# Performance work log

Hardware: AMD Instinct MI355X
Metric: run time of the kernel (lower is better)

## Reference

```python
import jax, jax.numpy as jnp
import numpy as np

ALPHA = 4.0  # spikingjelly surrogate.Sigmoid default
TAU = 2.0    # LIFNode default

@jax.custom_vjp
def spike(x):
    return (x >= 0).astype(x.dtype)

def _spike_fwd(x):
    return spike(x), x

def _spike_bwd(x, g):
    s = jax.nn.sigmoid(ALPHA * x)
    return (g * ALPHA * s * (1.0 - s),)

spike.defvjp(_spike_fwd, _spike_bwd)

def lif(x_seq, v_th):
    # multi-step LIF over leading time dim; decay_input=True, v_reset=0 (hard reset)
    def step(v, x):
        v = v + (x - v) / TAU
        s = spike(v - v_th)
        return v * (1.0 - s), s
    _, s_seq = jax.lax.scan(step, jnp.zeros_like(x_seq[0]), x_seq)
    return s_seq

def bn_c(x, gamma, beta, mean, var, eps=1e-5):
    # eval-mode BatchNorm1d over channel axis 2 of [T,N,C,V]
    inv = (gamma / jnp.sqrt(var + eps))[None, None, :, None]
    return (x - mean[None, None, :, None]) * inv + beta[None, None, :, None]

def conv1x1(x, w):
    # 1x1 Conv1d == channel mixing: w [Cout,Cin], x [T,N,C,V]
    return jnp.einsum('oc,tncv->tnov', w, x)

def setup_inputs() -> dict:
    key = jax.random.key(0)
    T, N, C, V = 4, 512, 256, 25
    ks = jax.random.split(key, 24)
    def bn_params(k1, k2, k3, k4):
        return (jax.random.uniform(k1, (C,)) * 0.5 + 0.75,
                jax.random.normal(k2, (C,)) * 0.1,
                jax.random.normal(k3, (C,)) * 0.1,
                jax.random.uniform(k4, (C,)) * 0.5 + 0.5)
    x = jax.random.normal(ks[0], (T, N, C, V), dtype=jnp.float32)
    s = 1.0 / np.sqrt(C)
    wq = jax.random.normal(ks[1], (C, C)) * s
    wk = jax.random.normal(ks[2], (C, C)) * s
    wv = jax.random.normal(ks[3], (C, C)) * s
    wp = jax.random.normal(ks[4], (C, C)) * s
    bp = jax.random.normal(ks[5], (C,)) * 0.02
    qg, qb, qm, qvar = bn_params(ks[6], ks[7], ks[8], ks[9])
    kg, kb, km, kvar = bn_params(ks[10], ks[11], ks[12], ks[13])
    vg, vb, vm, vvar = bn_params(ks[14], ks[15], ks[16], ks[17])
    pg, pb, pm, pvar = bn_params(ks[18], ks[19], ks[20], ks[21])
    return dict(x=x, wq=wq, wk=wk, wv=wv, wp=wp, bp=bp,
                qg=qg, qb=qb, qm=qm, qvar=qvar,
                kg=kg, kb=kb, km=km, kvar=kvar,
                vg=vg, vb=vb, vm=vm, vvar=vvar,
                pg=pg, pb=pb, pm=pm, pvar=pvar)

def reference(x, wq, wk, wv, wp, bp, qg, qb, qm, qvar, kg, kb, km, kvar,
              vg, vb, vm, vvar, pg, pb, pm, pvar):
    T, N, C, V = x.shape
    H = 8
    D = C // H
    scale = 0.125

    def branch(w, g, b, m, var):
        s = lif(bn_c(conv1x1(x, w), g, b, m, var), 1.0)       # [T,N,C,V]
        # -> [T,N,V,C] -> [T,N,V,H,D] -> [T,N,H,V,D]
        return jnp.transpose(s, (0, 1, 3, 2)).reshape(T, N, V, H, D).transpose(0, 1, 3, 2, 4)

    q = branch(wq, qg, qb, qm, qvar)
    k = branch(wk, kg, kb, km, kvar)
    v = branch(wv, vg, vb, vm, vvar)

    attn = jnp.einsum('tnhvd,tnhwd->tnhvw', q, k)            # binary spike attn, no softmax
    y = jnp.einsum('tnhvw,tnhwd->tnhvd', attn, v) * scale    # [T,N,H,V,D]
    y = y.transpose(0, 1, 2, 4, 3).reshape(T, N, C, V)       # transpose(3,4) then merge H*D=C
    y = lif(y, 0.5)                                          # attn_lif, v_threshold=0.5
    y = conv1x1(y, wp) + bp[None, None, :, None]             # proj_conv (bias=True)
    y = lif(bn_c(y, pg, pb, pm, pvar), 1.0)                  # proj_bn + proj_lif
    return y + x                                             # residual
```

## Files before the change

### kernel.cpp

```cpp
#include <hip/hip_runtime.h>
#include <cstdint>
#include <cstddef>

#define T_ 4
#define N_ 512
#define C_ 256
#define V_ 25
#define H_ 8

typedef _Float16 half8_t __attribute__((ext_vector_type(8)));
typedef float f32x16 __attribute__((ext_vector_type(16)));

__device__ __forceinline__ f32x16 mfma16(half8_t a, half8_t b, f32x16 c) {
  return __builtin_amdgcn_mfma_f32_32x32x16_f16(a, b, c, 0, 0, 0);
}

__global__ void kw_stage(const float* __restrict__ wq, const float* __restrict__ wk,
                         const float* __restrict__ wv, const float* __restrict__ wp,
                         const float* __restrict__ qg, const float* __restrict__ qvar,
                         const float* __restrict__ kg, const float* __restrict__ kvar,
                         const float* __restrict__ vg, const float* __restrict__ vvar,
                         const float* __restrict__ pg, const float* __restrict__ pvar,
                         _Float16* __restrict__ Wstg) {
  int i = blockIdx.x * 512 + threadIdx.x;
  int j = i & 7, lane = (i >> 3) & 63, rt = (i >> 9) & 3, m = (i >> 11) & 1;
  int s = (i >> 12) & 3, p = (i >> 14) & 3, c = i >> 16;
  int kt = p * 4 + s;
  int row = rt * 32 + (lane & 31);
  int k = kt * 16 + (lane >> 5) * 8 + j;
  const float *w, *g, *va;
  int grow;
  if (c < 6) {
    int br = c >> 1;
    w = br == 0 ? wq : br == 1 ? wk : wv;
    g = br == 0 ? qg : br == 1 ? kg : vg;
    va = br == 0 ? qvar : br == 1 ? kvar : vvar;
    grow = (c & 1) * 128 + row;
  } else {
    w = wp; g = pg; va = pvar;
    grow = (c - 6) * 128 + row;
  }
  float sc = g[grow] / sqrtf(va[grow] + 1e-5f);
  float wv_ = w[grow * 256 + k] * sc;
  _Float16 hi = (_Float16)wv_;
  Wstg[i] = (m == 0) ? hi : (_Float16)(wv_ - (float)hi);
}

__global__ void kx_stage(const float* __restrict__ x, _Float16* __restrict__ X16) {
  __shared__ float Xt[256 * 28];
  const int n = blockIdx.x, tid = threadIdx.x;
  for (int t = 0; t < 4; ++t) {
    __syncthreads();
    for (int i = tid; i < 6400; i += 256) {
      int k = i / 25, v = i - k * 25;
      Xt[k * 28 + v] = x[(size_t)(t * N_ + n) * 6400 + i];
    }
    __syncthreads();
    for (int jj = tid; jj < 800; jj += 256) {
      int kt = jj / 50, r = jj - kt * 50;
      int v = r >> 1, lkg = r & 1;
      int k0 = kt * 16 + lkg * 8;
      half8_t hi, lo;
#pragma unroll
      for (int e = 0; e < 8; ++e) {
        float f = Xt[(k0 + e) * 28 + v];
        _Float16 h = (_Float16)f;
        hi[e] = h;
        lo[e] = (_Float16)(f - (float)h);
      }
      int col = t * 25 + v;
      size_t bhi = ((((size_t)n * 2 + 0) * 16 + kt) * 100 + col) * 16 + lkg * 8;
      size_t blo = ((((size_t)n * 2 + 1) * 16 + kt) * 100 + col) * 16 + lkg * 8;
      *(half8_t*)(X16 + bhi) = hi;
      *(half8_t*)(X16 + blo) = lo;
    }
  }
}

#define STAGE_A(gidx, bufsel)                                                     \
  do {                                                                            \
    const _Float16* sp_ = Wstg + (size_t)(gidx) * 16384 + tid * 8;                \
    char* dp_ = Abuf + (bufsel) * 32768 + tid * 16;                               \
    __builtin_amdgcn_global_load_lds((const uint32_t*)(sp_),          (uint32_t*)(dp_),          16, 0, 0); \
    __builtin_amdgcn_global_load_lds((const uint32_t*)(sp_ + 4096),   (uint32_t*)(dp_ + 8192),   16, 0, 0); \
    __builtin_amdgcn_global_load_lds((const uint32_t*)(sp_ + 8192),   (uint32_t*)(dp_ + 16384),  16, 0, 0); \
    __builtin_amdgcn_global_load_lds((const uint32_t*)(sp_ + 12288),  (uint32_t*)(dp_ + 24576),  16, 0, 0); \
  } while (0)

#define MS_BYTE(colx, rowx) ((colx) * 256 + (((rowx) * 4) ^ (((colx) & 7) << 4)))

__launch_bounds__(512, 2)
__global__ void k1_mfma(const _Float16* __restrict__ X16, const _Float16* __restrict__ Wstg,
                        const float* __restrict__ qg, const float* __restrict__ qb,
                        const float* __restrict__ qm, const float* __restrict__ qvar,
                        const float* __restrict__ kg, const float* __restrict__ kb,
                        const float* __restrict__ km, const float* __restrict__ kvar,
                        const float* __restrict__ vg, const float* __restrict__ vb,
                        const float* __restrict__ vm, const float* __restrict__ vvar,
                        uint32_t* __restrict__ masks) {
  __shared__ __align__(16) char LDSb[65536 + 32768 + 512];
  char* Abuf = LDSb;
  char* MsB = LDSb + 65536;
  float* bic = (float*)(LDSb + 65536 + 32768);

  const int n = blockIdx.x, tid = threadIdx.x;
  const int lane = tid & 63, wid = tid >> 6;
  const int ks = wid & 1, cp = (wid >> 1) & 1, rt2 = wid >> 2;
  const int lr = lane & 31, lkg = lane >> 5;

  half8_t Bh[16], Bl[16];
#pragma unroll
  for (int ct = 0; ct < 2; ++ct) {
    int col = cp * 64 + ct * 32 + lr;
    if (col > 99) col = 99;
#pragma unroll
    for (int ktl = 0; ktl < 8; ++ktl) {
      int kt = ktl * 2 + ks;
      Bh[ct * 8 + ktl] = *(const half8_t*)(X16 + ((((size_t)n * 2 + 0) * 16 + kt) * 100 + col) * 16 + lkg * 8);
      Bl[ct * 8 + ktl] = *(const half8_t*)(X16 + ((((size_t)n * 2 + 1) * 16 + kt) * 100 + col) * 16 + lkg * 8);
    }
  }
  STAGE_A(0, 0);

  for (int c = 0; c < 6; ++c) {
    const int br = c >> 1;
    f32x16 acc00 = {}, acc01 = {}, acc10 = {}, acc11 = {};
#pragma unroll
    for (int p = 0; p < 4; ++p) {
      __syncthreads();
      if (p == 0 && tid < 128) {
        int ch = (c & 1) * 128 + tid;
        const float* g  = br == 0 ? qg : br == 1 ? kg : vg;
        const float* be = br == 0 ? qb : br == 1 ? kb : vb;
        const float* mu = br == 0 ? qm : br == 1 ? km : vm;
        const float* va = br == 0 ? qvar : br == 1 ? kvar : vvar;
        float sc = g[ch] / sqrtf(va[ch] + 1e-5f);
        bic[tid] = be[ch] - mu[ch] * sc;
      }
      int gnext = c * 4 + p + 1;
      if (gnext < 24) STAGE_A(gnext, (p + 1) & 1);
#pragma unroll
      for (int s2 = 0; s2 < 2; ++s2) {
        const int s = s2 * 2 + ks;
        const int bi = p * 2 + s2;
        const char* kb = Abuf + (p & 1) * 32768 + s * 8192 + (rt2 * 2) * 1024 + lane * 16;
        half8_t Ah0 = *(const half8_t*)(kb);
        half8_t Ah1 = *(const half8_t*)(kb + 1024);
        half8_t Al0 = *(const half8_t*)(kb + 4096);
        half8_t Al1 = *(const half8_t*)(kb + 4096 + 1024);
        __builtin_amdgcn_s_setprio(1);
        acc00 = mfma16(Ah0, Bh[bi], acc00);
        acc01 = mfma16(Ah0, Bh[8 + bi], acc01);
        acc10 = mfma16(Ah1, Bh[bi], acc10);
        acc11 = mfma16(Ah1, Bh[8 + bi], acc11);
        acc00 = mfma16(Ah0, Bl[bi], acc00);
        acc01 = mfma16(Ah0, Bl[8 + bi], acc01);
        acc10 = mfma16(Ah1, Bl[bi], acc10);
        acc11 = mfma16(Ah1, Bl[8 + bi], acc11);
        acc00 = mfma16(Al0, Bh[bi], acc00);
        acc01 = mfma16(Al0, Bh[8 + bi], acc01);
        acc10 = mfma16(Al1, Bh[bi], acc10);
        acc11 = mfma16(Al1, Bh[8 + bi], acc11);
        __builtin_amdgcn_s_setprio(0);
      }
    }

    __syncthreads();
    if (ks == 0) {
#pragma unroll
      for (int rsub = 0; rsub < 2; ++rsub) {
#pragma unroll
        for (int ct = 0; ct < 2; ++ct) {
          int col = cp * 64 + ct * 32 + lr;
          if (col < 100) {
            f32x16 A = rsub ? (ct ? acc11 : acc10) : (ct ? acc01 : acc00);
#pragma unroll
            for (int qq = 0; qq < 4; ++qq) {
              int rowb = (rt2 * 2 + rsub) * 32 + qq * 8 + lkg * 4;
              *(float4*)(MsB + MS_BYTE(col, rowb)) =
                  make_float4(A[qq * 4], A[qq * 4 + 1], A[qq * 4 + 2], A[qq * 4 + 3]);
            }
          }
        }
      }
    }
    __syncthreads();
    if (ks == 1) {
#pragma unroll
      for (int rsub = 0; rsub < 2; ++rsub) {
#pragma unroll
        for (int ct = 0; ct < 2; ++ct) {
          int col = cp * 64 + ct * 32 + lr;
          if (col < 100) {
            f32x16 A = rsub ? (ct ? acc11 : acc10) : (ct ? acc01 : acc00);
#pragma unroll
            for (int qq = 0; qq < 4; ++qq) {
              int rowb = (rt2 * 2 + rsub) * 32 + qq * 8 + lkg * 4;
              float4* mp = (float4*)(MsB + MS_BYTE(col, rowb));
              float4 old = *mp;
              *mp = make_float4(old.x + A[qq * 4], old.y + A[qq * 4 + 1],
                                old.z + A[qq * 4 + 2], old.w + A[qq * 4 + 3]);
            }
          }
        }
      }
    }
    __syncthreads();
    const int d = lane & 31, hl = lane >> 5;
    for (int it = 0; it < 7; ++it) {
      int task = it * 16 + wid * 2 + hl;
      bool valid = task < 100;
      int hg = valid ? task / 25 : 0;
      int v = valid ? task - hg * 25 : 0;
      int row = hg * 32 + d;
      float bicv = bic[row];
      float st = 0.0f;
#pragma unroll
      for (int t = 0; t < 4; ++t) {
        int colx = t * 25 + v;
        float cu = *(const float*)(MsB + MS_BYTE(colx, row)) + bicv;
        st += (cu - st) * 0.5f;
        bool sb = valid && (st >= 1.0f);
        if (st >= 1.0f) st = 0.0f;
        unsigned long long b = __ballot(sb);
        if (valid && (lane == 0 || lane == 32)) {
          uint32_t wd = (lane == 0) ? (uint32_t)b : (uint32_t)(b >> 32);
          masks[((((size_t)t * N_ + n) * 3 + br) * H_ + (c & 1) * 4 + hg) * V_ + v] = wd;
        }
      }
    }
  }
}

__launch_bounds__(64)
__global__ void k2_attn(const uint32_t* __restrict__ masks, uint32_t* __restrict__ mask2) {
  __shared__ uint32_t qs[T_][V_], ks_[T_][V_], vs[T_][V_];
  const int n = blockIdx.x >> 3;
  const int h = blockIdx.x & 7;
  const int l = threadIdx.x;
  for (int i = l; i < T_ * 3 * V_; i += 64) {
    int t = i / (3 * V_);
    int r = i - t * (3 * V_);
    int br = r / V_;
    int v = r - br * V_;
    uint32_t w = masks[(((size_t)t * N_ + n) * 3 + br) * (H_ * V_) + h * V_ + v];
    if (br == 0) qs[t][v] = w;
    else if (br == 1) ks_[t][v] = w;
    else vs[t][v] = w;
  }
  __syncthreads();
  const int hi = l >> 5, d = l & 31;
  for (int vv = 0; vv < 13; ++vv) {
    int v = vv * 2 + hi;
    bool valid = (v < V_);
    int vc = valid ? v : 0;
    float st = 0.0f;
#pragma unroll
    for (int t = 0; t < 4; ++t) {
      int y = 0;
      uint32_t qmw = qs[t][vc];
#pragma unroll
      for (int w = 0; w < V_; ++w) {
        int a = __popc(qmw & ks_[t][w]);
        y += a * (int)((vs[t][w] >> d) & 1u);
      }
      float yf = 0.125f * (float)y;
      st += (yf - st) * 0.5f;
      bool s = valid && (st >= 0.5f);
      if (st >= 0.5f) st = 0.0f;
      unsigned long long b = __ballot(s);
      if (valid && (l == 0 || l == 32)) {
        uint32_t wd = (l == 0) ? (uint32_t)b : (uint32_t)(b >> 32);
        mask2[(((size_t)t * N_ + n) * V_ + v) * H_ + h] = wd;
      }
    }
  }
}

__launch_bounds__(512, 2)
__global__ void k3_mfma(const float* __restrict__ x, const _Float16* __restrict__ Wstg,
                        const uint32_t* __restrict__ mask2, const float* __restrict__ bp,
                        const float* __restrict__ pg, const float* __restrict__ pb,
                        const float* __restrict__ pm, const float* __restrict__ pvar,
                        float* __restrict__ out) {
  __shared__ __align__(16) char LDSb[65536 + 32768 + 512 + 3200];
  char* Abuf = LDSb;
  char* MsB = LDSb + 65536;
  float* bic = (float*)(LDSb + 65536 + 32768);
  uint32_t* m2s = (uint32_t*)(LDSb + 65536 + 32768 + 512);

  const int n = blockIdx.x, tid = threadIdx.x;
  const int lane = tid & 63, wid = tid >> 6;
  const int rt = wid & 3, cp = wid >> 2;
  const int lr = lane & 31, lkg = lane >> 5;

  for (int i = tid; i < 800; i += 512) {
    int t = i / 200, r = i - t * 200;
    m2s[i] = mask2[(size_t)(t * N_ + n) * 200 + r];
  }
  __syncthreads();

  half8_t Bb[32];
#pragma unroll
  for (int ct = 0; ct < 2; ++ct) {
    int col = cp * 64 + ct * 32 + lr;
    bool valid = col < 100;
    int cc = valid ? col : 0;
    int t = cc / 25, v = cc - t * 25;
#pragma unroll
    for (int kt = 0; kt < 16; ++kt) {
#pragma unroll
      for (int jj = 0; jj < 8; ++jj) {
        int k = kt * 16 + lkg * 8 + jj;
        uint32_t bit = (m2s[t * 200 + v * 8 + (k >> 5)] >> (k & 31)) & 1u;
        Bb[ct * 16 + kt][jj] = (valid && bit) ? (_Float16)1.0f : (_Float16)0.0f;
      }
    }
  }
  STAGE_A(24, 0);

  for (int c = 0; c < 2; ++c) {
    f32x16 acc0 = {}, acc1 = {};
#pragma unroll
    for (int p = 0; p < 4; ++p) {
      __syncthreads();
      if (p == 0 && tid < 128) {
        int ch = c * 128 + tid;
        float sc = pg[ch] / sqrtf(pvar[ch] + 1e-5f);
        bic[tid] = fmaf(bp[ch] - pm[ch], sc, pb[ch]);
      }
      int gnext = (6 + c) * 4 + p + 1;
      if (gnext < 32) STAGE_A(gnext, (p + 1) & 1);
#pragma unroll
      for (int s = 0; s < 4; ++s) {
        const char* kb = Abuf + (p & 1) * 32768 + s * 8192 + rt * 1024 + lane * 16;
        half8_t Ahi = *(const half8_t*)(kb);
        half8_t Alo = *(const half8_t*)(kb + 4096);
        const int kt = p * 4 + s;
        __builtin_amdgcn_s_setprio(1);
        acc0 = mfma16(Ahi, Bb[kt], acc0);
        acc1 = mfma16(Ahi, Bb[16 + kt], acc1);
        acc0 = mfma16(Alo, Bb[kt], acc0);
        acc1 = mfma16(Alo, Bb[16 + kt], acc1);
        __builtin_amdgcn_s_setprio(0);
      }
    }

    __syncthreads();
#pragma unroll
    for (int ct = 0; ct < 2; ++ct) {
      int col = cp * 64 + ct * 32 + lr;
      if (col < 100) {
        f32x16 A = ct ? acc1 : acc0;
#pragma unroll
        for (int qq = 0; qq < 4; ++qq) {
          int rowb = rt * 32 + qq * 8 + lkg * 4;
          *(float4*)(MsB + MS_BYTE(col, rowb)) =
              make_float4(A[qq * 4], A[qq * 4 + 1], A[qq * 4 + 2], A[qq * 4 + 3]);
        }
      }
    }
    __syncthreads();
    const int d = lane & 31, hl = lane >> 5;
    for (int it = 0; it < 7; ++it) {
      int task = it * 16 + wid * 2 + hl;
      bool valid = task < 100;
      int hg = valid ? task / 25 : 0;
      int v = valid ? task - hg * 25 : 0;
      int row = hg * 32 + d;
      float bicv = bic[row];
      float st = 0.0f;
#pragma unroll
      for (int t = 0; t < 4; ++t) {
        int colx = t * 25 + v;
        char* mp = MsB + MS_BYTE(colx, row);
        if (valid) {
          float cu = *(const float*)(mp) + bicv;
          st += (cu - st) * 0.5f;
          float sv = (st >= 1.0f) ? 1.0f : 0.0f;
          if (st >= 1.0f) st = 0.0f;
          *(float*)(mp) = sv;
        }
      }
    }
    __syncthreads();
    for (int ii = tid; ii < 12800; ii += 512) {
      int t = ii / 3200, r2 = ii - t * 3200;
      int cl = r2 / 25, v = r2 - cl * 25;
      int colx = t * 25 + v;
      float sv = *(const float*)(MsB + MS_BYTE(colx, cl));
      size_t go = (size_t)(t * N_ + n) * 6400 + (size_t)(c * 128 + cl) * 25 + v;
      out[go] = sv + x[go];
    }
  }
}

extern "C" void kernel_launch(void* const* d_in, const int* in_sizes, int n_in,
                              void* d_out, int out_size, void* d_ws, size_t ws_size,
                              hipStream_t stream) {
  const float* x    = (const float*)d_in[0];
  const float* wq   = (const float*)d_in[1];
  const float* wk   = (const float*)d_in[2];
  const float* wv   = (const float*)d_in[3];
  const float* wp   = (const float*)d_in[4];
  const float* bp   = (const float*)d_in[5];
  const float* qg   = (const float*)d_in[6];
  const float* qb   = (const float*)d_in[7];
  const float* qm   = (const float*)d_in[8];
  const float* qvar = (const float*)d_in[9];
  const float* kg   = (const float*)d_in[10];
  const float* kb   = (const float*)d_in[11];
  const float* km   = (const float*)d_in[12];
  const float* kvar = (const float*)d_in[13];
  const float* vg   = (const float*)d_in[14];
  const float* vb   = (const float*)d_in[15];
  const float* vm   = (const float*)d_in[16];
  const float* vvar = (const float*)d_in[17];
  const float* pg   = (const float*)d_in[18];
  const float* pb   = (const float*)d_in[19];
  const float* pm   = (const float*)d_in[20];
  const float* pvar = (const float*)d_in[21];

  _Float16* Wstg = (_Float16*)d_ws;
  _Float16* X16  = (_Float16*)d_ws + 524288;
  uint32_t* masks = (uint32_t*)((char*)d_ws + 1048576 + 52428800);
  uint32_t* mask2 = masks + 1228800;

  kw_stage<<<1024, 512, 0, stream>>>(wq, wk, wv, wp, qg, qvar, kg, kvar,
                                     vg, vvar, pg, pvar, Wstg);
  kx_stage<<<512, 256, 0, stream>>>(x, X16);
  k1_mfma<<<512, 512, 0, stream>>>(X16, Wstg, qg, qb, qm, qvar, kg, kb, km, kvar,
                                   vg, vb, vm, vvar, masks);
  k2_attn<<<4096, 64, 0, stream>>>(masks, mask2);
  k3_mfma<<<512, 512, 0, stream>>>(x, Wstg, mask2, bp, pg, pb, pm, pvar, (float*)d_out);
}
```

Measured before the change: 294.3 us.

## Triple-buffer A staging with explicit waitcnt barriers, stage masks in LDS, restructure attn loop

k1 moves from a double-buffered to a triple-buffered global_load_lds pipeline that issues stages two steps ahead. It replaces __syncthreads with explicit vmcnt waits plus raw barriers to cut synchronisation stalls. BN bias for all six chunks is precomputed once into LDS, and spike masks are collected in LDS and written out coalesced at the end. k2 is reordered so each k/v word loaded from LDS is reused across 13 query rows held in registers. The larger LDS footprint (about 140KB) may lower occupancy below the 2 blocks per CU the launch bounds ask for.

Measured after the change: 289.9 us. No clear change (-1.5%).

```diff
diff --git a/kernel.cpp b/kernel.cpp
--- a/kernel.cpp
+++ b/kernel.cpp
@@ -14,6 +14,13 @@
 __device__ __forceinline__ f32x16 mfma16(half8_t a, half8_t b, f32x16 c) {
   return __builtin_amdgcn_mfma_f32_32x32x16_f16(a, b, c, 0, 0, 0);
 }
+
+#define WAITV(n) asm volatile("s_waitcnt vmcnt(" #n ")" ::: "memory")
+#define BAR_A()  do { __builtin_amdgcn_s_barrier(); __builtin_amdgcn_sched_barrier(0); } while (0)
+#define BAR_B()  do { asm volatile("" ::: "memory"); __builtin_amdgcn_s_barrier(); \
+                      __builtin_amdgcn_sched_barrier(0); } while (0)
+#define EPI_BAR() do { asm volatile("s_waitcnt lgkmcnt(0)" ::: "memory"); \
+                       __builtin_amdgcn_s_barrier(); __builtin_amdgcn_sched_barrier(0); } while (0)
 
 __global__ void kw_stage(const float* __restrict__ wq, const float* __restrict__ wk,
                          const float* __restrict__ wv, const float* __restrict__ wp,
@@ -98,16 +105,28 @@
                         const float* __restrict__ vg, const float* __restrict__ vb,
                         const float* __restrict__ vm, const float* __restrict__ vvar,
                         uint32_t* __restrict__ masks) {
-  __shared__ __align__(16) char LDSb[65536 + 32768 + 512];
+  __shared__ __align__(16) char LDSb[143744];
   char* Abuf = LDSb;
-  char* MsB = LDSb + 65536;
-  float* bic = (float*)(LDSb + 65536 + 32768);
+  char* MsB  = LDSb + 98304;
+  float* bicL = (float*)(LDSb + 131072);
+  uint32_t* mkL = (uint32_t*)(LDSb + 134144);
 
   const int n = blockIdx.x, tid = threadIdx.x;
   const int lane = tid & 63, wid = tid >> 6;
   const int ks = wid & 1, cp = (wid >> 1) & 1, rt2 = wid >> 2;
   const int lr = lane & 31, lkg = lane >> 5;
 
+  for (int i = tid; i < 768; i += 512) {
+    int cc = i >> 7, row = i & 127;
+    int br = cc >> 1, ch = (cc & 1) * 128 + row;
+    const float* g  = br == 0 ? qg : br == 1 ? kg : vg;
+    const float* be = br == 0 ? qb : br == 1 ? kb : vb;
+    const float* mu = br == 0 ? qm : br == 1 ? km : vm;
+    const float* va = br == 0 ? qvar : br == 1 ? kvar : vvar;
+    float sc = g[ch] / sqrtf(va[ch] + 1e-5f);
+    bicL[i] = be[ch] - mu[ch] * sc;
+  }
+
   half8_t Bh[16], Bl[16];
 #pragma unroll
   for (int ct = 0; ct < 2; ++ct) {
@@ -120,30 +139,29 @@
       Bl[ct * 8 + ktl] = *(const half8_t*)(X16 + ((((size_t)n * 2 + 1) * 16 + kt) * 100 + col) * 16 + lkg * 8);
     }
   }
+  __builtin_amdgcn_sched_barrier(0);
+  WAITV(0);
   STAGE_A(0, 0);
+  STAGE_A(1, 1);
+  STAGE_A(2, 2);
 
   for (int c = 0; c < 6; ++c) {
     const int br = c >> 1;
     f32x16 acc00 = {}, acc01 = {}, acc10 = {}, acc11 = {};
 #pragma unroll
     for (int p = 0; p < 4; ++p) {
-      __syncthreads();
-      if (p == 0 && tid < 128) {
-        int ch = (c & 1) * 128 + tid;
-        const float* g  = br == 0 ? qg : br == 1 ? kg : vg;
-        const float* be = br == 0 ? qb : br == 1 ? kb : vb;
-        const float* mu = br == 0 ? qm : br == 1 ? km : vm;
-        const float* va = br == 0 ? qvar : br == 1 ? kvar : vvar;
-        float sc = g[ch] / sqrtf(va[ch] + 1e-5f);
-        bic[tid] = be[ch] - mu[ch] * sc;
-      }
-      int gnext = c * 4 + p + 1;
-      if (gnext < 24) STAGE_A(gnext, (p + 1) & 1);
+      if (c < 5) { WAITV(8); }
+      else {
+        if (p < 2) { WAITV(8); } else if (p == 2) { WAITV(4); } else { WAITV(0); }
+      }
+      BAR_A();
+      const int bsel = (c + p) % 3;
+      const char* bufb = Abuf + bsel * 32768;
 #pragma unroll
       for (int s2 = 0; s2 < 2; ++s2) {
         const int s = s2 * 2 + ks;
         const int bi = p * 2 + s2;
-        const char* kb = Abuf + (p & 1) * 32768 + s * 8192 + (rt2 * 2) * 1024 + lane * 16;
+        const char* kb = bufb + s * 8192 + (rt2 * 2) * 1024 + lane * 16;
         half8_t Ah0 = *(const half8_t*)(kb);
         half8_t Ah1 = *(const half8_t*)(kb + 1024);
         half8_t Al0 = *(const half8_t*)(kb + 4096);
@@ -163,9 +181,11 @@
         acc11 = mfma16(Al1, Bh[8 + bi], acc11);
         __builtin_amdgcn_s_setprio(0);
       }
-    }
-
-    __syncthreads();
+      BAR_B();
+      int gn = c * 4 + p + 3;
+      if (gn < 24) STAGE_A(gn, bsel);
+    }
+
     if (ks == 0) {
 #pragma unroll
       for (int rsub = 0; rsub < 2; ++rsub) {
@@ -184,7 +204,7 @@
         }
       }
     }
-    __syncthreads();
+    EPI_BAR();
     if (ks == 1) {
 #pragma unroll
       for (int rsub = 0; rsub < 2; ++rsub) {
@@ -205,7 +225,7 @@
         }
       }
     }
-    __syncthreads();
+    EPI_BAR();
     const int d = lane & 31, hl = lane >> 5;
     for (int it = 0; it < 7; ++it) {
       int task = it * 16 + wid * 2 + hl;
@@ -213,7 +233,7 @@
       int hg = valid ? task / 25 : 0;
       int v = valid ? task - hg * 25 : 0;
       int row = hg * 32 + d;
-      float bicv = bic[row];
+      float bicv = bicL[c * 128 + row];
       float st = 0.0f;
 #pragma unroll
       for (int t = 0; t < 4; ++t) {
@@ -225,10 +245,16 @@
         unsigned long long b = __ballot(sb);
         if (valid && (lane == 0 || lane == 32)) {
           uint32_t wd = (lane == 0) ? (uint32_t)b : (uint32_t)(b >> 32);
-          masks[((((size_t)t * N_ + n) * 3 + br) * H_ + (c & 1) * 4 + hg) * V_ + v] = wd;
+          mkL[t * 600 + br * 200 + ((c & 1) * 4 + hg) * 25 + v] = wd;
         }
       }
     }
+  }
+
+  EPI_BAR();
+  for (int i = tid; i < 2400; i += 512) {
+    int t = i / 600, r = i - t * 600;
+    masks[(size_t)(t * N_ + n) * 600 + r] = mkL[i];
   }
 }
 
@@ -250,24 +276,33 @@
   }
   __syncthreads();
   const int hi = l >> 5, d = l & 31;
-  for (int vv = 0; vv < 13; ++vv) {
-    int v = vv * 2 + hi;
-    bool valid = (v < V_);
-    int vc = valid ? v : 0;
-    float st = 0.0f;
-#pragma unroll
-    for (int t = 0; t < 4; ++t) {
-      int y = 0;
-      uint32_t qmw = qs[t][vc];
-#pragma unroll
-      for (int w = 0; w < V_; ++w) {
-        int a = __popc(qmw & ks_[t][w]);
-        y += a * (int)((vs[t][w] >> d) & 1u);
-      }
-      float yf = 0.125f * (float)y;
-      st += (yf - st) * 0.5f;
-      bool s = valid && (st >= 0.5f);
-      if (st >= 0.5f) st = 0.0f;
+  float st[13];
+#pragma unroll
+  for (int vv = 0; vv < 13; ++vv) st[vv] = 0.0f;
+#pragma unroll
+  for (int t = 0; t < 4; ++t) {
+    uint32_t q[13];
+    int y[13];
+#pragma unroll
+    for (int vv = 0; vv < 13; ++vv) {
+      int v = vv * 2 + hi;
+      q[vv] = qs[t][v < V_ ? v : 0];
+      y[vv] = 0;
+    }
+    for (int w = 0; w < V_; ++w) {
+      uint32_t kw = ks_[t][w];
+      int vb = (int)((vs[t][w] >> d) & 1u);
+#pragma unroll
+      for (int vv = 0; vv < 13; ++vv) y[vv] += __popc(q[vv] & kw) * vb;
+    }
+#pragma unroll
+    for (int vv = 0; vv < 13; ++vv) {
+      int v = vv * 2 + hi;
+      bool valid = (v < V_);
+      float yf = 0.125f * (float)y[vv];
+      st[vv] += (yf - st[vv]) * 0.5f;
+      bool s = valid && (st[vv] >= 0.5f);
+      if (st[vv] >= 0.5f) st[vv] = 0.0f;
       unsigned long long b = __ballot(s);
       if (valid && (l == 0 || l == 32)) {
         uint32_t wd = (l == 0) ? (uint32_t)b : (uint32_t)(b >> 32);
```

## Fuse x staging, QKV conv, spike attention and projection into one kernel

Applied to the files above, without the earlier changes.

Merges kx_stage, k1_mfma, k2_attn and k3_mfma into a single per-sample kernel. x is converted to hi/lo fp16 straight into registers, and spike masks and attention outputs stay in LDS, so the global round-trips for X16, masks and mask2 and three launches are gone. Weight tiles are now double-buffered in registers from global memory instead of staged into LDS with global_load_lds, which cuts LDS use and barriers. In exchange, each lane reloads weights from L2 and the attention work runs on only 512 blocks instead of 4096.

Result: faster. 282.5 us (-4.0%).

```diff
diff --git a/kernel.cpp b/kernel.cpp
--- a/kernel.cpp
+++ b/kernel.cpp
@@ -46,122 +46,114 @@
   Wstg[i] = (m == 0) ? hi : (_Float16)(wv_ - (float)hi);
 }
 
-__global__ void kx_stage(const float* __restrict__ x, _Float16* __restrict__ X16) {
-  __shared__ float Xt[256 * 28];
-  const int n = blockIdx.x, tid = threadIdx.x;
-  for (int t = 0; t < 4; ++t) {
-    __syncthreads();
-    for (int i = tid; i < 6400; i += 256) {
-      int k = i / 25, v = i - k * 25;
-      Xt[k * 28 + v] = x[(size_t)(t * N_ + n) * 6400 + i];
-    }
-    __syncthreads();
-    for (int jj = tid; jj < 800; jj += 256) {
-      int kt = jj / 50, r = jj - kt * 50;
-      int v = r >> 1, lkg = r & 1;
-      int k0 = kt * 16 + lkg * 8;
-      half8_t hi, lo;
-#pragma unroll
-      for (int e = 0; e < 8; ++e) {
-        float f = Xt[(k0 + e) * 28 + v];
-        _Float16 h = (_Float16)f;
-        hi[e] = h;
-        lo[e] = (_Float16)(f - (float)h);
-      }
-      int col = t * 25 + v;
-      size_t bhi = ((((size_t)n * 2 + 0) * 16 + kt) * 100 + col) * 16 + lkg * 8;
-      size_t blo = ((((size_t)n * 2 + 1) * 16 + kt) * 100 + col) * 16 + lkg * 8;
-      *(half8_t*)(X16 + bhi) = hi;
-      *(half8_t*)(X16 + blo) = lo;
-    }
-  }
-}
-
-#define STAGE_A(gidx, bufsel)                                                     \
-  do {                                                                            \
-    const _Float16* sp_ = Wstg + (size_t)(gidx) * 16384 + tid * 8;                \
-    char* dp_ = Abuf + (bufsel) * 32768 + tid * 16;                               \
-    __builtin_amdgcn_global_load_lds((const uint32_t*)(sp_),          (uint32_t*)(dp_),          16, 0, 0); \
-    __builtin_amdgcn_global_load_lds((const uint32_t*)(sp_ + 4096),   (uint32_t*)(dp_ + 8192),   16, 0, 0); \
-    __builtin_amdgcn_global_load_lds((const uint32_t*)(sp_ + 8192),   (uint32_t*)(dp_ + 16384),  16, 0, 0); \
-    __builtin_amdgcn_global_load_lds((const uint32_t*)(sp_ + 12288),  (uint32_t*)(dp_ + 24576),  16, 0, 0); \
+#define MS_BYTE(colx, rowx) ((colx) * 256 + (((rowx) * 4) ^ (((colx) & 7) << 4)))
+
+#define QKV_LD(AH0, AH1, AL0, AL1, cc, gg)                                            \
+  do {                                                                                \
+    const _Float16* bp_ = Wstg + ((size_t)((cc) * 4 + ((gg) >> 1)) << 14) +           \
+                          ((size_t)((((gg) & 1) * 2 + ks)) << 12) +                   \
+                          ((rt2 * 2) << 9) + (lane << 3);                             \
+    AH0 = *(const half8_t*)(bp_);                                                     \
+    AH1 = *(const half8_t*)(bp_ + 512);                                               \
+    AL0 = *(const half8_t*)(bp_ + 2048);                                              \
+    AL1 = *(const half8_t*)(bp_ + 2048 + 512);                                        \
   } while (0)
 
-#define MS_BYTE(colx, rowx) ((colx) * 256 + (((rowx) * 4) ^ (((colx) & 7) << 4)))
+#define QKV_MMA(AH0, AH1, AL0, AL1, BI)                                               \
+  do {                                                                                \
+    __builtin_amdgcn_s_setprio(1);                                                    \
+    acc00 = mfma16(AH0, Bh[BI], acc00);                                               \
+    acc01 = mfma16(AH0, Bh[8 + BI], acc01);                                           \
+    acc10 = mfma16(AH1, Bh[BI], acc10);                                               \
+    acc11 = mfma16(AH1, Bh[8 + BI], acc11);                                           \
+    acc00 = mfma16(AH0, Bl[BI], acc00);                                               \
+    acc01 = mfma16(AH0, Bl[8 + BI], acc01);                                           \
+    acc10 = mfma16(AH1, Bl[BI], acc10);                                               \
+    acc11 = mfma16(AH1, Bl[8 + BI], acc11);                                           \
+    acc00 = mfma16(AL0, Bh[BI], acc00);                                               \
+    acc01 = mfma16(AL0, Bh[8 + BI], acc01);                                           \
+    acc10 = mfma16(AL1, Bh[BI], acc10);                                               \
+    acc11 = mfma16(AL1, Bh[8 + BI], acc11);                                           \
+    __builtin_amdgcn_s_setprio(0);                                                    \
+  } while (0)
+
+#define PRJ_LD(AHI, ALO, cc, kk)                                                      \
+  do {                                                                                \
+    const _Float16* bp_ = Wstg + ((size_t)(24 + (cc) * 4 + ((kk) >> 2)) << 14) +      \
+                          ((size_t)((kk) & 3) << 12) + (rt3 << 9) + (lane << 3);      \
+    AHI = *(const half8_t*)(bp_);                                                     \
+    ALO = *(const half8_t*)(bp_ + 2048);                                              \
+  } while (0)
 
 __launch_bounds__(512, 2)
-__global__ void k1_mfma(const _Float16* __restrict__ X16, const _Float16* __restrict__ Wstg,
-                        const float* __restrict__ qg, const float* __restrict__ qb,
-                        const float* __restrict__ qm, const float* __restrict__ qvar,
-                        const float* __restrict__ kg, const float* __restrict__ kb,
-                        const float* __restrict__ km, const float* __restrict__ kvar,
-                        const float* __restrict__ vg, const float* __restrict__ vb,
-                        const float* __restrict__ vm, const float* __restrict__ vvar,
-                        uint32_t* __restrict__ masks) {
-  __shared__ __align__(16) char LDSb[65536 + 32768 + 512];
-  char* Abuf = LDSb;
-  char* MsB = LDSb + 65536;
-  float* bic = (float*)(LDSb + 65536 + 32768);
+__global__ void k1_fused(const float* __restrict__ x, const _Float16* __restrict__ Wstg,
+                         const float* __restrict__ qg, const float* __restrict__ qb,
+                         const float* __restrict__ qm, const float* __restrict__ qvar,
+                         const float* __restrict__ kg, const float* __restrict__ kb,
+                         const float* __restrict__ km, const float* __restrict__ kvar,
+                         const float* __restrict__ vg, const float* __restrict__ vb,
+                         const float* __restrict__ vm, const float* __restrict__ vvar,
+                         const float* __restrict__ bp, const float* __restrict__ pg,
+                         const float* __restrict__ pb, const float* __restrict__ pm,
+                         const float* __restrict__ pvar, float* __restrict__ out) {
+  __shared__ __align__(16) char LDSb[48640];
+  char* MsB = LDSb;
+  float* bicL = (float*)(LDSb + 32768);
+  uint32_t* mkL = (uint32_t*)(LDSb + 35840);
+  uint32_t* m2L = (uint32_t*)(LDSb + 45440);
 
   const int n = blockIdx.x, tid = threadIdx.x;
   const int lane = tid & 63, wid = tid >> 6;
   const int ks = wid & 1, cp = (wid >> 1) & 1, rt2 = wid >> 2;
   const int lr = lane & 31, lkg = lane >> 5;
 
+  for (int i = tid; i < 768; i += 512) {
+    int cc = i >> 7, row = i & 127;
+    int br = cc >> 1, ch = (cc & 1) * 128 + row;
+    const float* g  = br == 0 ? qg : br == 1 ? kg : vg;
+    const float* be = br == 0 ? qb : br == 1 ? kb : vb;
+    const float* mu = br == 0 ? qm : br == 1 ? km : vm;
+    const float* va = br == 0 ? qvar : br == 1 ? kvar : vvar;
+    float sc = g[ch] / sqrtf(va[ch] + 1e-5f);
+    bicL[i] = be[ch] - mu[ch] * sc;
+  }
+
   half8_t Bh[16], Bl[16];
 #pragma unroll
   for (int ct = 0; ct < 2; ++ct) {
     int col = cp * 64 + ct * 32 + lr;
-    if (col > 99) col = 99;
+    bool valid = col < 100;
+    int cc = valid ? col : 0;
+    int t = cc / 25, v = cc - t * 25;
+    const float* xb = x + (size_t)(t * N_ + n) * 6400 + v;
 #pragma unroll
     for (int ktl = 0; ktl < 8; ++ktl) {
-      int kt = ktl * 2 + ks;
-      Bh[ct * 8 + ktl] = *(const half8_t*)(X16 + ((((size_t)n * 2 + 0) * 16 + kt) * 100 + col) * 16 + lkg * 8);
-      Bl[ct * 8 + ktl] = *(const half8_t*)(X16 + ((((size_t)n * 2 + 1) * 16 + kt) * 100 + col) * 16 + lkg * 8);
-    }
-  }
-  STAGE_A(0, 0);
-
+      int k0 = (ktl * 2 + ks) * 16 + lkg * 8;
+#pragma unroll
+      for (int e = 0; e < 8; ++e) {
+        float f = valid ? xb[(k0 + e) * 25] : 0.0f;
+        _Float16 h = (_Float16)f;
+        Bh[ct * 8 + ktl][e] = h;
+        Bl[ct * 8 + ktl][e] = (_Float16)(f - (float)h);
+      }
+    }
+  }
+  __syncthreads();
+
+  half8_t a0h0, a0h1, a0l0, a0l1, a1h0, a1h1, a1l0, a1l1;
+  QKV_LD(a0h0, a0h1, a0l0, a0l1, 0, 0);
   for (int c = 0; c < 6; ++c) {
     const int br = c >> 1;
     f32x16 acc00 = {}, acc01 = {}, acc10 = {}, acc11 = {};
 #pragma unroll
-    for (int p = 0; p < 4; ++p) {
-      __syncthreads();
-      if (p == 0 && tid < 128) {
-        int ch = (c & 1) * 128 + tid;
-        const float* g  = br == 0 ? qg : br == 1 ? kg : vg;
-        const float* be = br == 0 ? qb : br == 1 ? kb : vb;
-        const float* mu = br == 0 ? qm : br == 1 ? km : vm;
-        const float* va = br == 0 ? qvar : br == 1 ? kvar : vvar;
-        float sc = g[ch] / sqrtf(va[ch] + 1e-5f);
-        bic[tid] = be[ch] - mu[ch] * sc;
-      }
-      int gnext = c * 4 + p + 1;
-      if (gnext < 24) STAGE_A(gnext, (p + 1) & 1);
-#pragma unroll
-      for (int s2 = 0; s2 < 2; ++s2) {
-        const int s = s2 * 2 + ks;
-        const int bi = p * 2 + s2;
-        const char* kb = Abuf + (p & 1) * 32768 + s * 8192 + (rt2 * 2) * 1024 + lane * 16;
-        half8_t Ah0 = *(const half8_t*)(kb);
-        half8_t Ah1 = *(const half8_t*)(kb + 1024);
-        half8_t Al0 = *(const half8_t*)(kb + 4096);
-        half8_t Al1 = *(const half8_t*)(kb + 4096 + 1024);
-        __builtin_amdgcn_s_setprio(1);
-        acc00 = mfma16(Ah0, Bh[bi], acc00);
-        acc01 = mfma16(Ah0, Bh[8 + bi], acc01);
-        acc10 = mfma16(Ah1, Bh[bi], acc10);
-        acc11 = mfma16(Ah1, Bh[8 + bi], acc11);
-        acc00 = mfma16(Ah0, Bl[bi], acc00);
-        acc01 = mfma16(Ah0, Bl[8 + bi], acc01);
-        acc10 = mfma16(Ah1, Bl[bi], acc10);
-        acc11 = mfma16(Ah1, Bl[8 + bi], acc11);
-        acc00 = mfma16(Al0, Bh[bi], acc00);
-        acc01 = mfma16(Al0, Bh[8 + bi], acc01);
-        acc10 = mfma16(Al1, Bh[bi], acc10);
-        acc11 = mfma16(Al1, Bh[8 + bi], acc11);
-        __builtin_amdgcn_s_setprio(0);
+    for (int g = 0; g < 8; ++g) {
+      if ((g & 1) == 0) {
+        if (g < 7) QKV_LD(a1h0, a1h1, a1l0, a1l1, c, g + 1);
+        QKV_MMA(a0h0, a0h1, a0l0, a0l1, g);
+      } else {
+        if (g < 7) QKV_LD(a0h0, a0h1, a0l0, a0l1, c, g + 1);
+        else if (c < 5) QKV_LD(a0h0, a0h1, a0l0, a0l1, c + 1, 0);
+        QKV_MMA(a1h0, a1h1, a1l0, a1l1, g);
       }
     }
 
@@ -213,7 +205,7 @@
       int hg = valid ? task / 25 : 0;
       int v = valid ? task - hg * 25 : 0;
       int row = hg * 32 + d;
-      float bicv = bic[row];
+      float bicv = bicL[c * 128 + row];
       float st = 0.0f;
 #pragma unroll
       for (int t = 0; t < 4; ++t) {
@@ -225,85 +217,57 @@
         unsigned long long b = __ballot(sb);
         if (valid && (lane == 0 || lane == 32)) {
           uint32_t wd = (lane == 0) ? (uint32_t)b : (uint32_t)(b >> 32);
-          masks[((((size_t)t * N_ + n) * 3 + br) * H_ + (c & 1) * 4 + hg) * V_ + v] = wd;
-        }
-      }
-    }
-  }
-}
-
-__launch_bounds__(64)
-__global__ void k2_attn(const uint32_t* __restrict__ masks, uint32_t* __restrict__ mask2) {
-  __shared__ uint32_t qs[T_][V_], ks_[T_][V_], vs[T_][V_];
-  const int n = blockIdx.x >> 3;
-  const int h = blockIdx.x & 7;
-  const int l = threadIdx.x;
-  for (int i = l; i < T_ * 3 * V_; i += 64) {
-    int t = i / (3 * V_);
-    int r = i - t * (3 * V_);
-    int br = r / V_;
-    int v = r - br * V_;
-    uint32_t w = masks[(((size_t)t * N_ + n) * 3 + br) * (H_ * V_) + h * V_ + v];
-    if (br == 0) qs[t][v] = w;
-    else if (br == 1) ks_[t][v] = w;
-    else vs[t][v] = w;
+          mkL[t * 600 + br * 200 + ((c & 1) * 4 + hg) * 25 + v] = wd;
+        }
+      }
+    }
   }
   __syncthreads();
-  const int hi = l >> 5, d = l & 31;
-  for (int vv = 0; vv < 13; ++vv) {
-    int v = vv * 2 + hi;
-    bool valid = (v < V_);
-    int vc = valid ? v : 0;
-    float st = 0.0f;
+
+  {
+    const int h = wid, hi2 = lane >> 5, d = lane & 31;
+    float st2[13];
+#pragma unroll
+    for (int vv = 0; vv < 13; ++vv) st2[vv] = 0.0f;
 #pragma unroll
     for (int t = 0; t < 4; ++t) {
-      int y = 0;
-      uint32_t qmw = qs[t][vc];
-#pragma unroll
+      uint32_t q[13];
+      int y[13];
+#pragma unroll
+      for (int vv = 0; vv < 13; ++vv) {
+        int v = vv * 2 + hi2;
+        q[vv] = mkL[t * 600 + h * 25 + (v < V_ ? v : 0)];
+        y[vv] = 0;
+      }
       for (int w = 0; w < V_; ++w) {
-        int a = __popc(qmw & ks_[t][w]);
-        y += a * (int)((vs[t][w] >> d) & 1u);
-      }
-      float yf = 0.125f * (float)y;
-      st += (yf - st) * 0.5f;
-      bool s = valid && (st >= 0.5f);
-      if (st >= 0.5f) st = 0.0f;
-      unsigned long long b = __ballot(s);
-      if (valid && (l == 0 || l == 32)) {
-        uint32_t wd = (l == 0) ? (uint32_t)b : (uint32_t)(b >> 32);
-        mask2[(((size_t)t * N_ + n) * V_ + v) * H_ + h] = wd;
-      }
-    }
-  }
-}
-
-__launch_bounds__(512, 2)
-__global__ void k3_mfma(const float* __restrict__ x, const _Float16* __restrict__ Wstg,
-                        const uint32_t* __restrict__ mask2, const float* __restrict__ bp,
-                        const float* __restrict__ pg, const float* __restrict__ pb,
-                        const float* __restrict__ pm, const float* __restrict__ pvar,
-                        float* __restrict__ out) {
-  __shared__ __align__(16) char LDSb[65536 + 32768 + 512 + 3200];
-  char* Abuf = LDSb;
-  char* MsB = LDSb + 65536;
-  float* bic = (float*)(LDSb + 65536 + 32768);
-  uint32_t* m2s = (uint32_t*)(LDSb + 65536 + 32768 + 512);
-
-  const int n = blockIdx.x, tid = threadIdx.x;
-  const int lane = tid & 63, wid = tid >> 6;
-  const int rt = wid & 3, cp = wid >> 2;
-  const int lr = lane & 31, lkg = lane >> 5;
-
-  for (int i = tid; i < 800; i += 512) {
-    int t = i / 200, r = i - t * 200;
-    m2s[i] = mask2[(size_t)(t * N_ + n) * 200 + r];
+        uint32_t kw2 = mkL[t * 600 + 200 + h * 25 + w];
+        int vb = (int)((mkL[t * 600 + 400 + h * 25 + w] >> d) & 1u);
+#pragma unroll
+        for (int vv = 0; vv < 13; ++vv) y[vv] += __popc(q[vv] & kw2) * vb;
+      }
+#pragma unroll
+      for (int vv = 0; vv < 13; ++vv) {
+        int v = vv * 2 + hi2;
+        bool valid = (v < V_);
+        float yf = 0.125f * (float)y[vv];
+        st2[vv] += (yf - st2[vv]) * 0.5f;
+        bool s = valid && (st2[vv] >= 0.5f);
+        if (st2[vv] >= 0.5f) st2[vv] = 0.0f;
+        unsigned long long b = __ballot(s);
+        if (valid && (lane == 0 || lane == 32)) {
+          uint32_t wd = (lane == 0) ? (uint32_t)b : (uint32_t)(b >> 32);
+          m2L[t * 200 + v * 8 + h] = wd;
+        }
+      }
+    }
   }
   __syncthreads();
 
+  const int rt3 = wid & 3, cp3 = wid >> 2;
   half8_t Bb[32];
 #pragma unroll
   for (int ct = 0; ct < 2; ++ct) {
-    int col = cp * 64 + ct * 32 + lr;
+    int col = cp3 * 64 + ct * 32 + lr;
     bool valid = col < 100;
     int cc = valid ? col : 0;
     int t = cc / 25, v = cc - t * 25;
@@ -312,49 +276,51 @@
 #pragma unroll
       for (int jj = 0; jj < 8; ++jj) {
         int k = kt * 16 + lkg * 8 + jj;
-        uint32_t bit = (m2s[t * 200 + v * 8 + (k >> 5)] >> (k & 31)) & 1u;
+        uint32_t bit = (m2L[t * 200 + v * 8 + (k >> 5)] >> (k & 31)) & 1u;
         Bb[ct * 16 + kt][jj] = (valid && bit) ? (_Float16)1.0f : (_Float16)0.0f;
       }
     }
   }
-  STAGE_A(24, 0);
-
+  if (tid < 256) {
+    float sc = pg[tid] / sqrtf(pvar[tid] + 1e-5f);
+    bicL[tid] = fmaf(bp[tid] - pm[tid], sc, pb[tid]);
+  }
+
+  half8_t p0h, p0l, p1h, p1l;
+  PRJ_LD(p0h, p0l, 0, 0);
   for (int c = 0; c < 2; ++c) {
     f32x16 acc0 = {}, acc1 = {};
 #pragma unroll
-    for (int p = 0; p < 4; ++p) {
-      __syncthreads();
-      if (p == 0 && tid < 128) {
-        int ch = c * 128 + tid;
-        float sc = pg[ch] / sqrtf(pvar[ch] + 1e-5f);
-        bic[tid] = fmaf(bp[ch] - pm[ch], sc, pb[ch]);
-      }
-      int gnext = (6 + c) * 4 + p + 1;
-      if (gnext < 32) STAGE_A(gnext, (p + 1) & 1);
-#pragma unroll
-      for (int s = 0; s < 4; ++s) {
-        const char* kb = Abuf + (p & 1) * 32768 + s * 8192 + rt * 1024 + lane * 16;
-        half8_t Ahi = *(const half8_t*)(kb);
-        half8_t Alo = *(const half8_t*)(kb + 4096);
-        const int kt = p * 4 + s;
+    for (int kt = 0; kt < 16; ++kt) {
+      if ((kt & 1) == 0) {
+        if (kt < 15) PRJ_LD(p1h, p1l, c, kt + 1);
         __builtin_amdgcn_s_setprio(1);
-        acc0 = mfma16(Ahi, Bb[kt], acc0);
-        acc1 = mfma16(Ahi, Bb[16 + kt], acc1);
-        acc0 = mfma16(Alo, Bb[kt], acc0);
-        acc1 = mfma16(Alo, Bb[16 + kt], acc1);
+        acc0 = mfma16(p0h, Bb[kt], acc0);
+        acc1 = mfma16(p0h, Bb[16 + kt], acc1);
+        acc0 = mfma16(p0l, Bb[kt], acc0);
+        acc1 = mfma16(p0l, Bb[16 + kt], acc1);
         __builtin_amdgcn_s_setprio(0);
+      } else {
+        if (kt < 15) PRJ_LD(p0h, p0l, c, kt + 1);
+        else if (c < 1) PRJ_LD(p0h, p0l, 1, 0);
+        __builtin_amdgcn_s_setprio(1);
+        acc0 = mfma16(p1h, Bb[kt], acc0);
+        acc1 = mfma16(p1h, Bb[16 + kt], acc1);
+        acc0 = mfma16(p1l, Bb[kt], acc0);
+        acc1 = mfma16(p1l, Bb[16 + kt], acc1);
+        __builtin_amdgcn_s_setprio(0);
       }
     }
 
     __syncthreads();
 #pragma unroll
     for (int ct = 0; ct < 2; ++ct) {
-      int col = cp * 64 + ct * 32 + lr;
+      int col = cp3 * 64 + ct * 32 + lr;
       if (col < 100) {
         f32x16 A = ct ? acc1 : acc0;
 #pragma unroll
         for (int qq = 0; qq < 4; ++qq) {
-          int rowb = rt * 32 + qq * 8 + lkg * 4;
+          int rowb = rt3 * 32 + qq * 8 + lkg * 4;
           *(float4*)(MsB + MS_BYTE(col, rowb)) =
               make_float4(A[qq * 4], A[qq * 4 + 1], A[qq * 4 + 2], A[qq * 4 + 3]);
         }
@@ -368,7 +334,7 @@
       int hg = valid ? task / 25 : 0;
       int v = valid ? task - hg * 25 : 0;
       int row = hg * 32 + d;
-      float bicv = bic[row];
+      float bicv = bicL[c * 128 + row];
       float st = 0.0f;
 #pragma unroll
       for (int t = 0; t < 4; ++t) {
@@ -422,15 +388,10 @@
   const float* pvar = (const float*)d_in[21];
 
   _Float16* Wstg = (_Float16*)d_ws;
-  _Float16* X16  = (_Float16*)d_ws + 524288;
-  uint32_t* masks = (uint32_t*)((char*)d_ws + 1048576 + 52428800);
-  uint32_t* mask2 = masks + 1228800;
 
   kw_stage<<<1024, 512, 0, stream>>>(wq, wk, wv, wp, qg, qvar, kg, kvar,
                                      vg, vvar, pg, pvar, Wstg);
-  kx_stage<<<512, 256, 0, stream>>>(x, X16);
-  k1_mfma<<<512, 512, 0, stream>>>(X16, Wstg, qg, qb, qm, qvar, kg, kb, km, kvar,
-                                   vg, vb, vm, vvar, masks);
-  k2_attn<<<4096, 64, 0, stream>>>(masks, mask2);
-  k3_mfma<<<512, 512, 0, stream>>>(x, Wstg, mask2, bp, pg, pb, pm, pvar, (float*)d_out);
+  k1_fused<<<512, 512, 0, stream>>>(x, Wstg, qg, qb, qm, qvar, kg, kb, km, kvar,
+                                    vg, vb, vm, vvar, bp, pg, pb, pm, pvar,
+                                    (float*)d_out);
 }
```
